# Kernel tuning notes

Hardware: AMD Instinct MI355X
Metric: run time of the kernel (lower is better)

The kernel has to match this reference:

```python
import jax, jax.numpy as jnp
import numpy as np

EMBED_DIM = 256
NUM_CLASSES = 100000
BATCH = 1024
MARGIN = 0.2
SCALE = 30.0
EPS = 1e-07


def setup_inputs() -> dict:
    key = jax.random.key(0)
    k1, k2, k3 = jax.random.split(key, 3)
    embeddings = jax.random.normal(k1, (BATCH, EMBED_DIM), dtype=jnp.float32)
    # xavier_normal_ init for weight [num_classes, embed_dim]
    std = float(np.sqrt(2.0 / (NUM_CLASSES + EMBED_DIM)))
    weight = jax.random.normal(k2, (NUM_CLASSES, EMBED_DIM), dtype=jnp.float32) * std
    labels = jax.random.randint(k3, (BATCH,), 0, NUM_CLASSES, dtype=jnp.int64)
    return {"embeddings": embeddings, "weight": weight, "labels": labels}


def _l2_normalize(x, axis):
    # matches F.normalize(dim=..) with default eps=1e-12
    norm = jnp.linalg.norm(x, axis=axis, keepdims=True)
    return x / jnp.maximum(norm, 1e-12)


def reference(embeddings, weight, labels):
    emb_n = _l2_normalize(embeddings, axis=1)          # [B, D]
    w_n = _l2_normalize(weight, axis=1)                # [C, D]
    cos_theta = jnp.clip(emb_n @ w_n.T, -1.0 + EPS, 1.0 - EPS)  # [B, C]
    theta = jnp.arccos(cos_theta)
    target_mask = jax.nn.one_hot(labels, NUM_CLASSES, dtype=jnp.bool_)
    theta_m = jnp.where(target_mask, theta + MARGIN, theta)
    logits = SCALE * jnp.cos(theta_m)                  # [B, C]
    logp = jax.nn.log_softmax(logits, axis=1)
    loss = -jnp.mean(jnp.take_along_axis(logp, labels[:, None], axis=1))
    acc = jnp.mean((jnp.argmax(logits, axis=1) == labels).astype(jnp.float32))
    return (loss, acc)
```

## Files before the change

### kernel.cpp

```cpp
#include <hip/hip_runtime.h>
#include <stdint.h>

#define DIM    256
#define BATCH  1024
#define NCLS   100000
#define NCT    250
#define TPG    25
#define CPG    400
#define RG     8
#define WGTBLK 6250
#define CLIPV  0.9999999f
#define COSM   0.98006657784124163f
#define SINM   0.19866933079506122f
#define K30L2E 43.280851226668903f
#define SQK    6.5788184f

typedef __attribute__((ext_vector_type(4))) float floatx4;
typedef __attribute__((ext_vector_type(2))) unsigned long ulong2v;

#define EMBF_OFF 0
#define WGTF_OFF (256 * 1024)
#define TL_OFF   (WGTF_OFF + (size_t)NCLS * DIM)
#define PU_OFF   (TL_OFF + 4096)
#define SP_OFF   (PU_OFF + 4096)
#define MP_OFF   (SP_OFF + (size_t)NCT * BATCH * 4)

__global__ __launch_bounds__(256) void k_prep(
        const float* __restrict__ emb, const float* __restrict__ wgt,
        const int* __restrict__ labels,
        unsigned char* __restrict__ emb8f, unsigned char* __restrict__ wgt8f,
        float* __restrict__ TL, float* __restrict__ PU) {
    const int b = blockIdx.x;
    const int tid = threadIdx.x;
    const int w = tid >> 6, l = tid & 63;
    const int sub = w * 4 + (l >> 4);
    const int l16 = l & 15;

    if (b < 64 + WGTBLK) {
        const bool isEmb = (b < 64);
        const float* src = isEmb ? emb : wgt;
        unsigned char* dst = isEmb ? emb8f : wgt8f;
        const int r = (isEmb ? b : b - 64) * 16 + sub;
        const int r16 = r & 15;
        float v[16];
        float ss = 0.f;
        const float* rp = src + (size_t)r * DIM + l16 * 16;
#pragma unroll
        for (int i = 0; i < 4; ++i) {
            float4 a = *(const float4*)(rp + i * 4);
            v[i*4+0]=a.x; v[i*4+1]=a.y; v[i*4+2]=a.z; v[i*4+3]=a.w;
            ss += a.x*a.x + a.y*a.y + a.z*a.z + a.w*a.w;
        }
#pragma unroll
        for (int k = 1; k < 16; k <<= 1) ss += __shfl_xor(ss, k);
        const float sc = SQK / fmaxf(sqrtf(ss), 1e-12f);
        unsigned char* tb = dst + (size_t)(r >> 4) * 4096;
#pragma unroll
        for (int h = 0; h < 2; ++h) {
            const int g = 2 * l16 + h;
            const int s = g >> 2, q = g & 3;
            int p0 = 0, p1 = 0;
            p0 = __builtin_amdgcn_cvt_pk_fp8_f32(v[h*8+0]*sc, v[h*8+1]*sc, p0, false);
            p0 = __builtin_amdgcn_cvt_pk_fp8_f32(v[h*8+2]*sc, v[h*8+3]*sc, p0, true);
            p1 = __builtin_amdgcn_cvt_pk_fp8_f32(v[h*8+4]*sc, v[h*8+5]*sc, p1, false);
            p1 = __builtin_amdgcn_cvt_pk_fp8_f32(v[h*8+6]*sc, v[h*8+7]*sc, p1, true);
            uint2 o; o.x = (unsigned)p0; o.y = (unsigned)p1;
            *(uint2*)(tb + (s >> 1) * 1024 + (r16 + 16 * q) * 16 + (s & 1) * 8) = o;
        }
    } else {
        const int r = (b - 64 - WGTBLK) * 16 + sub;
        const int lbl = labels[r];
        const float* ep = emb + (size_t)r * DIM + l16 * 16;
        const float* wp = wgt + (size_t)lbl * DIM + l16 * 16;
        float de = 0.f, dw = 0.f, dd = 0.f;
#pragma unroll
        for (int i = 0; i < 4; ++i) {
            float4 a = *(const float4*)(ep + i * 4);
            float4 bq = *(const float4*)(wp + i * 4);
            de += a.x*a.x + a.y*a.y + a.z*a.z + a.w*a.w;
            dw += bq.x*bq.x + bq.y*bq.y + bq.z*bq.z + bq.w*bq.w;
            dd += a.x*bq.x + a.y*bq.y + a.z*bq.z + a.w*bq.w;
        }
#pragma unroll
        for (int k = 1; k < 16; k <<= 1) {
            de += __shfl_xor(de, k); dw += __shfl_xor(dw, k); dd += __shfl_xor(dd, k);
        }
        if (l16 == 0) {
            float t = dd / (fmaxf(sqrtf(de), 1e-12f) * fmaxf(sqrtf(dw), 1e-12f));
            t = fminf(fmaxf(t, -CLIPV), CLIPV);
            PU[r] = exp2f(t * K30L2E);
            TL[r] = t * COSM - sqrtf(fmaxf(1.f - t * t, 0.f)) * SINM;
        }
    }
}

__global__ __launch_bounds__(256, 6) void k_main(
        const unsigned char* __restrict__ wgt8f,
        const unsigned char* __restrict__ emb8f,
        float* __restrict__ SP, unsigned* __restrict__ MP) {
    const int cg = blockIdx.x;
    const int rg = blockIdx.y;
    const int tid = threadIdx.x;
    const int w = tid >> 6, l = tid & 63;
    const int r16 = l & 15, q = l >> 4;
    const int rowbase = rg * 128 + w * 32;

    long af[2][8];
#pragma unroll
    for (int mt = 0; mt < 2; ++mt) {
        const ulong2v* ap =
            (const ulong2v*)(emb8f + (size_t)((rowbase >> 4) + mt) * 4096) + l;
#pragma unroll
        for (int p = 0; p < 4; ++p) {
            ulong2v v = ap[p * 64];
            af[mt][2*p]   = (long)v.x;
            af[mt][2*p+1] = (long)v.y;
        }
    }

    float sum[2][4] = {{0.f,0.f,0.f,0.f},{0.f,0.f,0.f,0.f}};
    float mx [2][4] = {{0.f,0.f,0.f,0.f},{0.f,0.f,0.f,0.f}};

    const ulong2v* bp = (const ulong2v*)(wgt8f + (size_t)(cg * TPG) * 4096) + l;
    for (int t = 0; t < TPG; ++t, bp += 256) {
        long bf[8];
#pragma unroll
        for (int p = 0; p < 4; ++p) {
            ulong2v v = bp[p * 64];
            bf[2*p]   = (long)v.x;
            bf[2*p+1] = (long)v.y;
        }
#pragma unroll
        for (int mt = 0; mt < 2; ++mt) {
            floatx4 acc = {0.f, 0.f, 0.f, 0.f};
#pragma unroll
            for (int s = 0; s < 8; ++s)
                acc = __builtin_amdgcn_mfma_f32_16x16x32_fp8_fp8(af[mt][s], bf[s], acc, 0, 0, 0);
#pragma unroll
            for (int r = 0; r < 4; ++r) {
                const float p = exp2f(acc[r]);
                sum[mt][r] += p;
                mx[mt][r] = fmaxf(mx[mt][r], p);
            }
        }
    }

#pragma unroll
    for (int k = 1; k < 16; k <<= 1)
#pragma unroll
        for (int mt = 0; mt < 2; ++mt)
#pragma unroll
            for (int r = 0; r < 4; ++r) {
                sum[mt][r] += __shfl_xor(sum[mt][r], k);
                mx[mt][r] = fmaxf(mx[mt][r], __shfl_xor(mx[mt][r], k));
            }
    if (r16 < 4) {
#pragma unroll
        for (int mt = 0; mt < 2; ++mt) {
            float sv = sum[mt][0], mv = mx[mt][0];
            if (r16 == 1) { sv = sum[mt][1]; mv = mx[mt][1]; }
            else if (r16 == 2) { sv = sum[mt][2]; mv = mx[mt][2]; }
            else if (r16 == 3) { sv = sum[mt][3]; mv = mx[mt][3]; }
            const int row = rowbase + mt * 16 + q * 4 + r16;
            SP[cg * BATCH + row] = sv;
            MP[cg * BATCH + row] = __float_as_uint(mv);
        }
    }
}

__global__ __launch_bounds__(256) void k_final(
        const float* __restrict__ SP, const unsigned* __restrict__ MP,
        const float* __restrict__ TL, const float* __restrict__ PU,
        float* __restrict__ out) {
    __shared__ float    ls[16][16];
    __shared__ unsigned lm[16][16];
    const int tid = threadIdx.x;
    const int r16 = tid & 15;
    const int c   = tid >> 4;
    const int row = blockIdx.x * 16 + r16;
    float s = 0.f;
    unsigned m = 0u;
    for (int b = c; b < NCT; b += 16) {
        s += SP[(size_t)b * BATCH + row];
        const unsigned v = MP[(size_t)b * BATCH + row];
        m = v > m ? v : m;
    }
    ls[c][r16] = s; lm[c][r16] = m;
    __syncthreads();
    float loss = 0.f, corr = 0.f;
    if (tid < 16) {
        float st = 0.f; unsigned mt = 0u;
#pragma unroll
        for (int i = 0; i < 16; ++i) {
            st += ls[i][tid];
            mt = lm[i][tid] > mt ? lm[i][tid] : mt;
        }
        const int r = blockIdx.x * 16 + tid;
        const float tl = TL[r];
        const float padj = exp2f(tl * K30L2E);
        st = st - PU[r] + padj;
        loss = logf(st) - 30.f * tl;
        corr = (padj >= __uint_as_float(mt)) ? 1.f : 0.f;
    }
#pragma unroll
    for (int k = 1; k < 16; k <<= 1) {
        loss += __shfl_xor(loss, k);
        corr += __shfl_xor(corr, k);
    }
    if (tid == 0) {
        atomicAdd(out + 0, loss * (1.f / 1024.f));
        atomicAdd(out + 1, corr * (1.f / 1024.f));
    }
}

extern "C" void kernel_launch(void* const* d_in, const int* in_sizes, int n_in,
                              void* d_out, int out_size, void* d_ws, size_t ws_size,
                              hipStream_t stream) {
    (void)in_sizes; (void)n_in; (void)out_size; (void)ws_size;
    const float* emb    = (const float*)d_in[0];
    const float* wgt    = (const float*)d_in[1];
    const int*   labels = (const int*)d_in[2];
    char* ws = (char*)d_ws;
    unsigned char* emb8f = (unsigned char*)(ws + EMBF_OFF);
    unsigned char* wgt8f = (unsigned char*)(ws + WGTF_OFF);
    float*    TL = (float*)(ws + TL_OFF);
    float*    PU = (float*)(ws + PU_OFF);
    float*    SP = (float*)(ws + SP_OFF);
    unsigned* MP = (unsigned*)(ws + MP_OFF);

    hipMemsetAsync(d_out, 0, 2 * sizeof(float), stream);
    k_prep<<<64 + WGTBLK + 64, 256, 0, stream>>>(emb, wgt, labels,
                                                 emb8f, wgt8f, TL, PU);
    k_main<<<dim3(NCT, RG), 256, 0, stream>>>(wgt8f, emb8f, SP, MP);
    k_final<<<64, 256, 0, stream>>>(SP, MP, TL, PU, (float*)d_out);
}
```

Measured before the change: 218.2 us.

## Pad classes to 256 tiles, interleave MFMA chains, use raw exp2

Pads the class count so the main grid has 256 column tiles instead of 250. The zero-filled padded rows produce logits of 0, and their exp2 contribution of 1 each (2400 total) is subtracted in the final kernel. The two MFMA accumulator chains are interleaved so the independent tiles overlap, and the loop is kept rolled. Library exp2f is replaced by the hardware builtin, and the occupancy hint drops from 6 to 5 waves. This adds extra FP8 conversion and matmul work for the padded rows and relies on the padded contributions being exactly 1.

```diff
diff --git a/kernel.cpp b/kernel.cpp
--- a/kernel.cpp
+++ b/kernel.cpp
@@ -4,11 +4,12 @@
 #define DIM    256
 #define BATCH  1024
 #define NCLS   100000
-#define NCT    250
+#define NCT    256
 #define TPG    25
-#define CPG    400
+#define NCLS_PAD (NCT * TPG * 16)
+#define PADC   2400.0f
 #define RG     8
-#define WGTBLK 6250
+#define WGTBLK (NCLS_PAD / 16)
 #define CLIPV  0.9999999f
 #define COSM   0.98006657784124163f
 #define SINM   0.19866933079506122f
@@ -20,7 +21,7 @@
 
 #define EMBF_OFF 0
 #define WGTF_OFF (256 * 1024)
-#define TL_OFF   (WGTF_OFF + (size_t)NCLS * DIM)
+#define TL_OFF   (WGTF_OFF + (size_t)NCLS_PAD * DIM)
 #define PU_OFF   (TL_OFF + 4096)
 #define SP_OFF   (PU_OFF + 4096)
 #define MP_OFF   (SP_OFF + (size_t)NCT * BATCH * 4)
@@ -40,16 +41,22 @@
         const bool isEmb = (b < 64);
         const float* src = isEmb ? emb : wgt;
         unsigned char* dst = isEmb ? emb8f : wgt8f;
+        const int nvalid = isEmb ? BATCH : NCLS;
         const int r = (isEmb ? b : b - 64) * 16 + sub;
         const int r16 = r & 15;
         float v[16];
         float ss = 0.f;
-        const float* rp = src + (size_t)r * DIM + l16 * 16;
-#pragma unroll
-        for (int i = 0; i < 4; ++i) {
-            float4 a = *(const float4*)(rp + i * 4);
-            v[i*4+0]=a.x; v[i*4+1]=a.y; v[i*4+2]=a.z; v[i*4+3]=a.w;
-            ss += a.x*a.x + a.y*a.y + a.z*a.z + a.w*a.w;
+        if (r < nvalid) {
+            const float* rp = src + (size_t)r * DIM + l16 * 16;
+#pragma unroll
+            for (int i = 0; i < 4; ++i) {
+                float4 a = *(const float4*)(rp + i * 4);
+                v[i*4+0]=a.x; v[i*4+1]=a.y; v[i*4+2]=a.z; v[i*4+3]=a.w;
+                ss += a.x*a.x + a.y*a.y + a.z*a.z + a.w*a.w;
+            }
+        } else {
+#pragma unroll
+            for (int i = 0; i < 16; ++i) v[i] = 0.f;
         }
 #pragma unroll
         for (int k = 1; k < 16; k <<= 1) ss += __shfl_xor(ss, k);
@@ -88,13 +95,13 @@
         if (l16 == 0) {
             float t = dd / (fmaxf(sqrtf(de), 1e-12f) * fmaxf(sqrtf(dw), 1e-12f));
             t = fminf(fmaxf(t, -CLIPV), CLIPV);
-            PU[r] = exp2f(t * K30L2E);
+            PU[r] = __builtin_amdgcn_exp2f(t * K30L2E);
             TL[r] = t * COSM - sqrtf(fmaxf(1.f - t * t, 0.f)) * SINM;
         }
     }
 }
 
-__global__ __launch_bounds__(256, 6) void k_main(
+__global__ __launch_bounds__(256, 5) void k_main(
         const unsigned char* __restrict__ wgt8f,
         const unsigned char* __restrict__ emb8f,
         float* __restrict__ SP, unsigned* __restrict__ MP) {
@@ -122,6 +129,7 @@
     float mx [2][4] = {{0.f,0.f,0.f,0.f},{0.f,0.f,0.f,0.f}};
 
     const ulong2v* bp = (const ulong2v*)(wgt8f + (size_t)(cg * TPG) * 4096) + l;
+#pragma unroll 1
     for (int t = 0; t < TPG; ++t, bp += 256) {
         long bf[8];
 #pragma unroll
@@ -130,18 +138,21 @@
             bf[2*p]   = (long)v.x;
             bf[2*p+1] = (long)v.y;
         }
-#pragma unroll
-        for (int mt = 0; mt < 2; ++mt) {
-            floatx4 acc = {0.f, 0.f, 0.f, 0.f};
-#pragma unroll
-            for (int s = 0; s < 8; ++s)
-                acc = __builtin_amdgcn_mfma_f32_16x16x32_fp8_fp8(af[mt][s], bf[s], acc, 0, 0, 0);
-#pragma unroll
-            for (int r = 0; r < 4; ++r) {
-                const float p = exp2f(acc[r]);
-                sum[mt][r] += p;
-                mx[mt][r] = fmaxf(mx[mt][r], p);
-            }
+        floatx4 acc0 = {0.f, 0.f, 0.f, 0.f};
+        floatx4 acc1 = {0.f, 0.f, 0.f, 0.f};
+#pragma unroll
+        for (int s = 0; s < 8; ++s) {
+            acc0 = __builtin_amdgcn_mfma_f32_16x16x32_fp8_fp8(af[0][s], bf[s], acc0, 0, 0, 0);
+            acc1 = __builtin_amdgcn_mfma_f32_16x16x32_fp8_fp8(af[1][s], bf[s], acc1, 0, 0, 0);
+        }
+#pragma unroll
+        for (int r = 0; r < 4; ++r) {
+            const float p0 = __builtin_amdgcn_exp2f(acc0[r]);
+            const float p1 = __builtin_amdgcn_exp2f(acc1[r]);
+            sum[0][r] += p0;
+            sum[1][r] += p1;
+            mx[0][r] = fmaxf(mx[0][r], p0);
+            mx[1][r] = fmaxf(mx[1][r], p1);
         }
     }
 
@@ -197,8 +208,8 @@
         }
         const int r = blockIdx.x * 16 + tid;
         const float tl = TL[r];
-        const float padj = exp2f(tl * K30L2E);
-        st = st - PU[r] + padj;
+        const float padj = __builtin_amdgcn_exp2f(tl * K30L2E);
+        st = st - PADC - PU[r] + padj;
         loss = logf(st) - 30.f * tl;
         corr = (padj >= __uint_as_float(mt)) ? 1.f : 0.f;
     }
```

After: 209.1 us. 1.04x faster.
